# Performance work log

Hardware: AMD Instinct MI355X
Metric: run time of the kernel (lower is better)

Reference implementation:

```python
import jax, jax.numpy as jnp
import numpy as np

Q_MIN, Q_MAX = -128.0, 127.0  # int8 range (brevitas signed, narrow_range=False)


def ste_round(x):
    # straight-through round (matches brevitas training semantics)
    return x + jax.lax.stop_gradient(jnp.round(x) - x)


def fake_quant(x, s):
    # per-tensor int8 quant-dequant: clamp(round(x/s), -128, 127) * s
    return jnp.clip(ste_round(x / s), Q_MIN, Q_MAX) * s


def conv2d(x, w):
    # NCHW x OIHW, stride 1, VALID padding (kernel (3,3), no padding arg in source)
    return jax.lax.conv_general_dilated(
        x, w, window_strides=(1, 1), padding='VALID',
        dimension_numbers=('NCHW', 'OIHW', 'NCHW'))


def setup_inputs() -> dict:
    key = jax.random.key(0)
    k = jax.random.split(key, 5)
    x = jax.random.normal(k[0], (32, 5, 512, 512), jnp.float32)
    w1 = jax.random.normal(k[1], (10, 5, 3, 3), jnp.float32) * 0.1
    b1 = jax.random.normal(k[2], (10,), jnp.float32) * 0.1
    w2 = jax.random.normal(k[3], (10, 10, 3, 3), jnp.float32) * 0.1
    b2 = jax.random.normal(k[4], (10,), jnp.float32) * 0.1
    # fixed-point (power-of-two) per-tensor scales
    s_in = jnp.full((1,), 2.0 ** -4, jnp.float32)
    s_w1 = jnp.full((1,), 2.0 ** -7, jnp.float32)
    s_o1 = jnp.full((1,), 2.0 ** -4, jnp.float32)
    s_w2 = jnp.full((1,), 2.0 ** -7, jnp.float32)
    s_o2 = jnp.full((1,), 2.0 ** -4, jnp.float32)
    return {"x": x, "w1": w1, "b1": b1, "w2": w2, "b2": b2,
            "s_in": s_in, "s_w1": s_w1, "s_o1": s_o1, "s_w2": s_w2, "s_o2": s_o2}


def reference(x, w1, b1, w2, b2, s_in, s_w1, s_o1, s_w2, s_o2):
    # QuantIdentity(Int8ActPerTensorFixedPoint)
    xq = fake_quant(x, s_in)
    # QuantConv2d #1: weight quant, bias quant (scale = in_scale*w_scale), output quant
    w1q = fake_quant(w1, s_w1)
    b1q = fake_quant(b1, s_in * s_w1)
    y = conv2d(xq, w1q) + b1q[None, :, None, None]  # [32,10,510,510]
    yq = fake_quant(y, s_o1)
    # QuantConv2d #2
    w2q = fake_quant(w2, s_w2)
    b2q = fake_quant(b2, s_o1 * s_w2)
    z = conv2d(yq, w2q) + b2q[None, :, None, None]  # [32,10,508,508]
    return fake_quant(z, s_o2)
```

## Files before the change

kernel.cpp:

```cpp
#include <hip/hip_runtime.h>


#define XQ_OFF   8192
#define YQ_OFF   41951488ULL

typedef int v4i __attribute__((ext_vector_type(4)));

__device__ __forceinline__ float qclamp(float v) {
    return fminf(fmaxf(v, -128.0f), 127.0f);
}

__device__ __forceinline__ int alignb(int hi, int lo, int sh) {
#if __has_builtin(__builtin_amdgcn_alignbyte)
    return __builtin_amdgcn_alignbyte(hi, lo, sh);
#else
    return (int)((((unsigned long long)(unsigned)hi << 32) | (unsigned)lo) >> (8 * sh));
#endif
}

__global__ __launch_bounds__(256) void prep_kernel(
    const float* __restrict__ w1, const float* __restrict__ b1,
    const float* __restrict__ w2, const float* __restrict__ b2,
    const float* __restrict__ s_in, const float* __restrict__ s_w1,
    const float* __restrict__ s_o1, const float* __restrict__ s_w2,
    const float* __restrict__ s_o2,
    float* __restrict__ consts, int* __restrict__ wA1, int* __restrict__ b1i,
    int* __restrict__ wA2, int* __restrict__ b2i)
{
    int t = threadIdx.x;
    float si = s_in[0], sw1 = s_w1[0], so1 = s_o1[0], sw2 = s_w2[0], so2 = s_o2[0];
    if (t == 0) {
        consts[0] = 1.0f / si;
        consts[1] = (si * sw1) / so1;
        consts[2] = (so1 * sw2) / so2;
        consts[3] = so2;
    }
    {
        int l = t >> 2, r = t & 3;
        int g = l >> 4, m = l & 15;
        int d = 4 * g + r;
        int val = 0;
        if (d < 15 && m < 10) {
            int c = d / 3, kh = d % 3;
            const float* src = w1 + (((m * 5 + c) * 3 + kh) * 3);
            int q0 = (int)qclamp(rintf(src[0] / sw1));
            int q1 = (int)qclamp(rintf(src[1] / sw1));
            int q2 = (int)qclamp(rintf(src[2] / sw1));
            val = (q0 & 255) | ((q1 & 255) << 8) | ((q2 & 255) << 16);
        }
        wA1[t] = val;
    }
    for (int i = t; i < 512; i += 256) {
        int l = i >> 3, r = i & 7;
        int g = l >> 4, m = l & 15;
        int f = r >> 2;
        int d = f * 16 + 4 * g + (r & 3);
        int val = 0;
        if (d < 30 && m < 10) {
            int c = d / 3, kh = d % 3;
            const float* src = w2 + (((m * 10 + c) * 3 + kh) * 3);
            int q0 = (int)qclamp(rintf(src[0] / sw2));
            int q1 = (int)qclamp(rintf(src[1] / sw2));
            int q2 = (int)qclamp(rintf(src[2] / sw2));
            val = (q0 & 255) | ((q1 & 255) << 8) | ((q2 & 255) << 16);
        }
        wA2[i] = val;
    }
    if (t < 16) {
        b1i[t] = (t < 10) ? (int)qclamp(rintf(b1[t] / (si * sw1))) : 0;
        b2i[t] = (t < 10) ? (int)qclamp(rintf(b2[t] / (so1 * sw2))) : 0;
    }
}

__global__ __launch_bounds__(256) void quant_x_kernel(
    const float4* __restrict__ x, const float* __restrict__ consts,
    int* __restrict__ xq, int n4)
{
    int i = blockIdx.x * 256 + threadIdx.x;
    if (i >= n4) return;
    float inv = consts[0];
    float4 v = x[i];
    int q0 = (int)qclamp(rintf(v.x * inv));
    int q1 = (int)qclamp(rintf(v.y * inv));
    int q2 = (int)qclamp(rintf(v.z * inv));
    int q3 = (int)qclamp(rintf(v.w * inv));
    xq[i] = (q0 & 255) | ((q1 & 255) << 8) | ((q2 & 255) << 16) | (q3 << 24);
}

__global__ __launch_bounds__(256) void conv1_mfma(
    const signed char* __restrict__ xq, const int* __restrict__ wA,
    const int* __restrict__ bi, const float* __restrict__ consts,
    signed char* __restrict__ yq)
{
    int lane = threadIdx.x & 63;
    int W = blockIdx.x * 4 + (threadIdx.x >> 6);
    int owt = W & 31;
    int rem = W >> 5;
    int ohc = rem % 17;
    int n = rem / 17;
    int g = lane >> 4, m = lane & 15;
    int ow0 = owt << 4;

    v4i a = ((const v4i*)wA)[lane];
    v4i cinit;
    #pragma unroll
    for (int r = 0; r < 4; ++r) cinit[r] = bi[4 * g + r];

    int koff[4];
    #pragma unroll
    for (int s = 0; s < 4; ++s) {
        int d = 4 * g + s;
        koff[s] = (d < 15) ? (d / 3) * 262144 + (d % 3) * 512 : 0;
    }
    int xoff = ow0 + (m & ~3);
    int sh = m & 3;
    int oh0 = ohc * 30;
    int base = n * (5 * 512 * 512) + oh0 * 512 + xoff;
    float cr1 = consts[1];
    bool owv = (ow0 + m) < 510;
    size_t sbase = (((size_t)(n * 10) * 510) + oh0) * 512 + ow0 + m;

    for (int i = 0; i < 30; ++i) {
        v4i b;
        #pragma unroll
        for (int s = 0; s < 4; ++s) {
            const int* p = (const int*)(xq + base + koff[s]);
            int u0 = p[0], u1 = p[1];
            b[s] = alignb(u1, u0, sh);
        }
        v4i acc = __builtin_amdgcn_mfma_i32_16x16x64_i8(a, b, cinit, 0, 0, 0);
        #pragma unroll
        for (int r = 0; r < 4; ++r) {
            int oc = 4 * g + r;
            if (oc < 10 && owv) {
                int q = (int)qclamp(rintf((float)acc[r] * cr1));
                yq[sbase + (size_t)oc * (510 * 512)] = (signed char)q;
            }
        }
        base += 512;
        sbase += 512;
    }
}

__global__ __launch_bounds__(256) void conv2_mfma(
    const signed char* __restrict__ yq, const int* __restrict__ wA,
    const int* __restrict__ bi, const float* __restrict__ consts,
    float* __restrict__ out)
{
    int lane = threadIdx.x & 63;
    int W = blockIdx.x * 4 + (threadIdx.x >> 6);
    int owt = W & 31;
    int ohc = (W >> 5) & 15;
    int n = W >> 9;
    int g = lane >> 4, m = lane & 15;
    int ow0 = owt << 4;

    const v4i* wA4 = (const v4i*)wA;
    v4i a0 = wA4[lane * 2 + 0];
    v4i a1 = wA4[lane * 2 + 1];
    v4i cinit;
    #pragma unroll
    for (int r = 0; r < 4; ++r) cinit[r] = bi[4 * g + r];

    int koff[8];
    #pragma unroll
    for (int s = 0; s < 8; ++s) {
        int d = (s >> 2) * 16 + 4 * g + (s & 3);
        koff[s] = (d < 30) ? (d / 3) * (510 * 512) + (d % 3) * 512 : 0;
    }
    int xoff = ow0 + (m & ~3);
    int sh = m & 3;
    int oh0 = ohc * 32;
    int base = n * (10 * 510 * 512) + oh0 * 512 + xoff;
    float cr2 = consts[2];
    float so  = consts[3];
    bool owv = (ow0 + m) < 508;
    size_t sbase = (((size_t)(n * 10) * 508) + oh0) * 508 + ow0 + m;
    int iters = (508 - oh0 < 32) ? (508 - oh0) : 32;

    for (int i = 0; i < iters; ++i) {
        v4i b0, b1v;
        #pragma unroll
        for (int s = 0; s < 4; ++s) {
            const int* p = (const int*)(yq + base + koff[s]);
            int u0 = p[0], u1 = p[1];
            b0[s] = alignb(u1, u0, sh);
        }
        #pragma unroll
        for (int s = 4; s < 8; ++s) {
            const int* p = (const int*)(yq + base + koff[s]);
            int u0 = p[0], u1 = p[1];
            b1v[s - 4] = alignb(u1, u0, sh);
        }
        v4i acc = __builtin_amdgcn_mfma_i32_16x16x64_i8(a0, b0, cinit, 0, 0, 0);
        acc = __builtin_amdgcn_mfma_i32_16x16x64_i8(a1, b1v, acc, 0, 0, 0);
        #pragma unroll
        for (int r = 0; r < 4; ++r) {
            int oc = 4 * g + r;
            if (oc < 10 && owv) {
                float v = qclamp(rintf((float)acc[r] * cr2)) * so;
                out[sbase + (size_t)oc * (508 * 508)] = v;
            }
        }
        base += 512;
        sbase += 508;
    }
}

extern "C" void kernel_launch(void* const* d_in, const int* in_sizes, int n_in,
                              void* d_out, int out_size, void* d_ws, size_t ws_size,
                              hipStream_t stream) {
    const float* x    = (const float*)d_in[0];
    const float* w1   = (const float*)d_in[1];
    const float* b1   = (const float*)d_in[2];
    const float* w2   = (const float*)d_in[3];
    const float* b2   = (const float*)d_in[4];
    const float* s_in = (const float*)d_in[5];
    const float* s_w1 = (const float*)d_in[6];
    const float* s_o1 = (const float*)d_in[7];
    const float* s_w2 = (const float*)d_in[8];
    const float* s_o2 = (const float*)d_in[9];

    char* ws = (char*)d_ws;
    float* consts = (float*)ws;
    int* wA1 = (int*)(ws + 256);
    int* b1i = (int*)(ws + 1280);
    int* wA2 = (int*)(ws + 2048);
    int* b2i = (int*)(ws + 4096);
    signed char* xqb = (signed char*)(ws + XQ_OFF);
    signed char* yqb = (signed char*)(ws + YQ_OFF);

    prep_kernel<<<1, 256, 0, stream>>>(w1, b1, w2, b2, s_in, s_w1, s_o1, s_w2, s_o2,
                                       consts, wA1, b1i, wA2, b2i);

    int n4 = 32 * 5 * 512 * 512 / 4;
    quant_x_kernel<<<(n4 + 255) / 256, 256, 0, stream>>>(
        (const float4*)x, consts, (int*)xqb, n4);

    conv1_mfma<<<4352, 256, 0, stream>>>(xqb, wA1, b1i, consts, yqb);

    conv2_mfma<<<4096, 256, 0, stream>>>(yqb, wA2, b2i, consts, (float*)d_out);
}
```

Baseline: 703.9 us.

## Stage input rows in LDS ring buffer for both int8 MFMA convolutions

Both convolution kernels now have each block cooperatively load a 4-row ring of input rows (all channels, 256+ columns) into shared memory. Each wave then builds its MFMA B operands from LDS for four 16-column tiles per output row, instead of every wave issuing redundant unaligned global loads per kernel-row offset. This targets redundant global/L2 traffic and the scattered byte loads of the old per-wave 16-column tiling. The cost is two __syncthreads per output row and a fixed block geometry with fewer, larger blocks.

```diff
diff --git a/kernel.cpp b/kernel.cpp
--- a/kernel.cpp
+++ b/kernel.cpp
@@ -92,54 +92,95 @@
     const int* __restrict__ bi, const float* __restrict__ consts,
     signed char* __restrict__ yq)
 {
-    int lane = threadIdx.x & 63;
-    int W = blockIdx.x * 4 + (threadIdx.x >> 6);
-    int owt = W & 31;
-    int rem = W >> 5;
-    int ohc = rem % 17;
-    int n = rem / 17;
+    int tid = threadIdx.x;
+    int b = blockIdx.x;
+    int rc = b & 31, wt = (b >> 5) & 1, n = b >> 6;
+    int oh0 = rc * 16;
+    int rows = 510 - oh0; if (rows > 16) rows = 16;
+    int ow0 = wt << 8;
+
+    __shared__ int lds[4 * 5 * 72];
+
+    int lane = tid & 63;
+    int w = tid >> 6;
     int g = lane >> 4, m = lane & 15;
-    int ow0 = owt << 4;
+    int sh = m & 3;
+    int wcol = w * 64;
 
     v4i a = ((const v4i*)wA)[lane];
     v4i cinit;
     #pragma unroll
     for (int r = 0; r < 4; ++r) cinit[r] = bi[4 * g + r];
 
-    int koff[4];
+    int khv[4], inv[4];
     #pragma unroll
-    for (int s = 0; s < 4; ++s) {
-        int d = 4 * g + s;
-        koff[s] = (d < 15) ? (d / 3) * 262144 + (d % 3) * 512 : 0;
-    }
-    int xoff = ow0 + (m & ~3);
-    int sh = m & 3;
-    int oh0 = ohc * 30;
-    int base = n * (5 * 512 * 512) + oh0 * 512 + xoff;
+    for (int j = 0; j < 4; ++j) {
+        int d = 4 * g + j;
+        int c = 0, kh = 0;
+        if (d < 15) { c = d / 3; kh = d % 3; }
+        khv[j] = kh;
+        inv[j] = c * 72 + ((wcol + (m & ~3)) >> 2);
+    }
+
+    const signed char* src = xq + (size_t)n * (5 * 512 * 512);
     float cr1 = consts[1];
-    bool owv = (ow0 + m) < 510;
-    size_t sbase = (((size_t)(n * 10) * 510) + oh0) * 512 + ow0 + m;
-
-    for (int i = 0; i < 30; ++i) {
-        v4i b;
+
+    #define STAGE1(ih_) do {                                                 \
+        int ih = (ih_);                                                      \
+        int slot = ih & 3;                                                   \
+        _Pragma("unroll")                                                    \
+        for (int pass = 0; pass < 2; ++pass) {                               \
+            int j = tid + pass * 256;                                        \
+            if (j < 340) {                                                   \
+                int c = j / 68;                                              \
+                int off = j - c * 68;                                        \
+                int col = ow0 + (off << 2);                                  \
+                if (col > 508) col = 508;                                    \
+                lds[(slot * 5 + c) * 72 + off] =                             \
+                    *(const int*)(src + c * 262144 + ih * 512 + col);        \
+            }                                                                \
+        }                                                                    \
+    } while (0)
+
+    STAGE1(oh0);
+    STAGE1(oh0 + 1);
+
+    for (int i = 0; i < rows; ++i) {
+        int oh = oh0 + i;
+        STAGE1(oh + 2);
+        __syncthreads();
+
+        int rsl[4];
         #pragma unroll
-        for (int s = 0; s < 4; ++s) {
-            const int* p = (const int*)(xq + base + koff[s]);
-            int u0 = p[0], u1 = p[1];
-            b[s] = alignb(u1, u0, sh);
+        for (int j = 0; j < 4; ++j)
+            rsl[j] = ((oh + khv[j]) & 3) * 360 + inv[j];
+
+        size_t sb = (size_t)(n * 10) * (510 * 512) + (size_t)oh * 512
+                  + (size_t)(ow0 + wcol + m);
+        #pragma unroll
+        for (int nt = 0; nt < 4; ++nt) {
+            v4i bb;
+            #pragma unroll
+            for (int j = 0; j < 4; ++j) {
+                const int* p = lds + rsl[j] + nt * 4;
+                int u0 = p[0], u1 = p[1];
+                bb[j] = alignb(u1, u0, sh);
+            }
+            v4i acc = __builtin_amdgcn_mfma_i32_16x16x64_i8(a, bb, cinit, 0, 0, 0);
+            int colv = ow0 + wcol + nt * 16 + m;
+            bool cv = colv < 510;
+            #pragma unroll
+            for (int r = 0; r < 4; ++r) {
+                int oc = 4 * g + r;
+                if (oc < 10 && cv) {
+                    int q = (int)qclamp(rintf((float)acc[r] * cr1));
+                    yq[sb + nt * 16 + (size_t)oc * (510 * 512)] = (signed char)q;
+                }
+            }
         }
-        v4i acc = __builtin_amdgcn_mfma_i32_16x16x64_i8(a, b, cinit, 0, 0, 0);
-        #pragma unroll
-        for (int r = 0; r < 4; ++r) {
-            int oc = 4 * g + r;
-            if (oc < 10 && owv) {
-                int q = (int)qclamp(rintf((float)acc[r] * cr1));
-                yq[sbase + (size_t)oc * (510 * 512)] = (signed char)q;
-            }
-        }
-        base += 512;
-        sbase += 512;
-    }
+        __syncthreads();
+    }
+    #undef STAGE1
 }
 
 __global__ __launch_bounds__(256) void conv2_mfma(
@@ -147,13 +188,20 @@
     const int* __restrict__ bi, const float* __restrict__ consts,
     float* __restrict__ out)
 {
-    int lane = threadIdx.x & 63;
-    int W = blockIdx.x * 4 + (threadIdx.x >> 6);
-    int owt = W & 31;
-    int ohc = (W >> 5) & 15;
-    int n = W >> 9;
+    int tid = threadIdx.x;
+    int b = blockIdx.x;
+    int rc = b & 31, wt = (b >> 5) & 1, n = b >> 6;
+    int oh0 = rc * 16;
+    int rows = 508 - oh0; if (rows > 16) rows = 16;
+    int ow0 = wt << 8;
+
+    __shared__ int lds[4 * 10 * 72];
+
+    int lane = tid & 63;
+    int w = tid >> 6;
     int g = lane >> 4, m = lane & 15;
-    int ow0 = owt << 4;
+    int sh = m & 3;
+    int wcol = w * 64;
 
     const v4i* wA4 = (const v4i*)wA;
     v4i a0 = wA4[lane * 2 + 0];
@@ -162,49 +210,82 @@
     #pragma unroll
     for (int r = 0; r < 4; ++r) cinit[r] = bi[4 * g + r];
 
-    int koff[8];
+    int khv[8], inv[8];
     #pragma unroll
     for (int s = 0; s < 8; ++s) {
         int d = (s >> 2) * 16 + 4 * g + (s & 3);
-        koff[s] = (d < 30) ? (d / 3) * (510 * 512) + (d % 3) * 512 : 0;
-    }
-    int xoff = ow0 + (m & ~3);
-    int sh = m & 3;
-    int oh0 = ohc * 32;
-    int base = n * (10 * 510 * 512) + oh0 * 512 + xoff;
+        int c = 0, kh = 0;
+        if (d < 30) { c = d / 3; kh = d % 3; }
+        khv[s] = kh;
+        inv[s] = c * 72 + ((wcol + (m & ~3)) >> 2);
+    }
+
+    const signed char* src = yq + (size_t)n * (10 * 510 * 512);
     float cr2 = consts[2];
     float so  = consts[3];
-    bool owv = (ow0 + m) < 508;
-    size_t sbase = (((size_t)(n * 10) * 508) + oh0) * 508 + ow0 + m;
-    int iters = (508 - oh0 < 32) ? (508 - oh0) : 32;
-
-    for (int i = 0; i < iters; ++i) {
-        v4i b0, b1v;
+
+    #define STAGE2(ih_) do {                                                 \
+        int ih = (ih_);                                                      \
+        int slot = ih & 3;                                                   \
+        _Pragma("unroll")                                                    \
+        for (int pass = 0; pass < 3; ++pass) {                               \
+            int j = tid + pass * 256;                                        \
+            if (j < 680) {                                                   \
+                int c = j / 68;                                              \
+                int off = j - c * 68;                                        \
+                int col = ow0 + (off << 2);                                  \
+                if (col > 508) col = 508;                                    \
+                lds[(slot * 10 + c) * 72 + off] =                            \
+                    *(const int*)(src + c * (510 * 512) + ih * 512 + col);   \
+            }                                                                \
+        }                                                                    \
+    } while (0)
+
+    STAGE2(oh0);
+    STAGE2(oh0 + 1);
+
+    for (int i = 0; i < rows; ++i) {
+        int oh = oh0 + i;
+        STAGE2(oh + 2);
+        __syncthreads();
+
+        int rsl[8];
         #pragma unroll
-        for (int s = 0; s < 4; ++s) {
-            const int* p = (const int*)(yq + base + koff[s]);
-            int u0 = p[0], u1 = p[1];
-            b0[s] = alignb(u1, u0, sh);
+        for (int s = 0; s < 8; ++s)
+            rsl[s] = ((oh + khv[s]) & 3) * 720 + inv[s];
+
+        size_t ob = (size_t)(n * 10) * (508 * 508) + (size_t)oh * 508;
+        #pragma unroll
+        for (int nt = 0; nt < 4; ++nt) {
+            v4i bb0, bb1;
+            #pragma unroll
+            for (int s = 0; s < 4; ++s) {
+                const int* p = lds + rsl[s] + nt * 4;
+                int u0 = p[0], u1 = p[1];
+                bb0[s] = alignb(u1, u0, sh);
+            }
+            #pragma unroll
+            for (int s = 4; s < 8; ++s) {
+                const int* p = lds + rsl[s] + nt * 4;
+                int u0 = p[0], u1 = p[1];
+                bb1[s - 4] = alignb(u1, u0, sh);
+            }
+            v4i acc = __builtin_amdgcn_mfma_i32_16x16x64_i8(a0, bb0, cinit, 0, 0, 0);
+            acc = __builtin_amdgcn_mfma_i32_16x16x64_i8(a1, bb1, acc, 0, 0, 0);
+            int colv = ow0 + wcol + nt * 16 + m;
+            bool cv = colv < 508;
+            #pragma unroll
+            for (int r = 0; r < 4; ++r) {
+                int oc = 4 * g + r;
+                if (oc < 10 && cv) {
+                    float v = qclamp(rintf((float)acc[r] * cr2)) * so;
+                    out[ob + (size_t)oc * (508 * 508) + colv] = v;
+                }
+            }
         }
-        #pragma unroll
-        for (int s = 4; s < 8; ++s) {
-            const int* p = (const int*)(yq + base + koff[s]);
-            int u0 = p[0], u1 = p[1];
-            b1v[s - 4] = alignb(u1, u0, sh);
-        }
-        v4i acc = __builtin_amdgcn_mfma_i32_16x16x64_i8(a0, b0, cinit, 0, 0, 0);
-        acc = __builtin_amdgcn_mfma_i32_16x16x64_i8(a1, b1v, acc, 0, 0, 0);
-        #pragma unroll
-        for (int r = 0; r < 4; ++r) {
-            int oc = 4 * g + r;
-            if (oc < 10 && owv) {
-                float v = qclamp(rintf((float)acc[r] * cr2)) * so;
-                out[sbase + (size_t)oc * (508 * 508)] = v;
-            }
-        }
-        base += 512;
-        sbase += 508;
-    }
+        __syncthreads();
+    }
+    #undef STAGE2
 }
 
 extern "C" void kernel_launch(void* const* d_in, const int* in_sizes, int n_in,
@@ -237,7 +318,7 @@
     quant_x_kernel<<<(n4 + 255) / 256, 256, 0, stream>>>(
         (const float4*)x, consts, (int*)xqb, n4);
 
-    conv1_mfma<<<4352, 256, 0, stream>>>(xqb, wA1, b1i, consts, yqb);
-
-    conv2_mfma<<<4096, 256, 0, stream>>>(yqb, wA2, b2i, consts, (float*)d_out);
-}
+    conv1_mfma<<<2048, 256, 0, stream>>>(xqb, wA1, b1i, consts, yqb);
+
+    conv2_mfma<<<2048, 256, 0, stream>>>(yqb, wA2, b2i, consts, (float*)d_out);
+}
```

Result: faster. 608.5 us (-13.6%).
